# Performance work log

Hardware: AMD Instinct MI355X
Metric: run time of the kernel (lower is better)

## Reference

```python
import jax, jax.numpy as jnp
import numpy as np

B, S, D, H = 2, 1024, 768, 12
HD = D // H          # head_dim = 64
DFF = 4 * D          # 3072
EPS = 1e-5


def _ln(x, g, b):
    m = x.mean(-1, keepdims=True)
    v = ((x - m) ** 2).mean(-1, keepdims=True)
    return (x - m) * jax.lax.rsqrt(v + EPS) * g + b


def setup_inputs() -> dict:
    key = jax.random.key(0)
    ks = jax.random.split(key, 8)
    w = lambda k, shape: jax.random.normal(k, shape, jnp.float32) * 0.02
    return {
        "inp": jax.random.normal(ks[0], (B, S, D), jnp.float32),
        "attention_mask": jnp.zeros((B, S), bool),  # True = masked out (filled with -inf)
        "rel_matrix": jax.random.randint(ks[1], (B, S, S), -1, 2, jnp.int32),  # values in {-1,0,1}
        "qkv_w": w(ks[2], (3 * D, D)),
        "rel_A": w(ks[3], (3, HD)),        # relative_position_emb_A.weight
        "o_w": w(ks[4], (D, D)),
        "w1": w(ks[5], (DFF, D)), "b1": jnp.zeros((DFF,), jnp.float32),
        "w2": w(ks[6], (D, DFF)), "b2": jnp.zeros((D,), jnp.float32),
        "ln1_g": jnp.ones((D,), jnp.float32), "ln1_b": jnp.zeros((D,), jnp.float32),
        "ln2_g": jnp.ones((D,), jnp.float32), "ln2_b": jnp.zeros((D,), jnp.float32),
    }


def reference(inp, attention_mask, rel_matrix, qkv_w, rel_A, o_w,
              w1, b1, w2, b2, ln1_g, ln1_b, ln2_g, ln2_b):
    x = _ln(inp, ln1_g, ln1_b)
    qkv = x @ qkv_w.T                                  # (B,S,3D)
    q, k, v = jnp.split(qkv, 3, axis=-1)
    heads = lambda t: t.reshape(B, S, H, HD).transpose(0, 2, 1, 3)  # (B,H,S,HD)
    q, k, v = heads(q), heads(k), heads(v)

    # q @ (k + rel_emb)^T without materializing k_aug:
    # q.k^T term plus per-(q,key) relative term gathered from q @ A^T.
    logits = jnp.einsum("bhqd,bhkd->bhqk", q, k)       # (B,H,S,S)
    r = jnp.einsum("bhqd,cd->bhqc", q, rel_A)          # (B,H,S,3)
    idx = (rel_matrix + 1).astype(jnp.int32)           # (B,S,S) in {0,1,2}
    rel = jnp.take_along_axis(r, jnp.broadcast_to(idx[:, None], (B, H, S, S)), axis=-1)
    logits = (logits + rel) / np.sqrt(HD).astype(np.float32)
    # masked_fill: -inf where mask is True
    logits = jnp.where(attention_mask[:, None, None, :], -jnp.inf, logits)

    attn = jax.nn.softmax(logits, axis=-1)
    out = jnp.einsum("bhqk,bhkd->bhqd", attn, v)
    out = out.transpose(0, 2, 1, 3).reshape(B, S, D)
    inp = inp + out @ o_w.T                            # residual (dropout=0)

    h = _ln(inp, ln2_g, ln2_b)
    mlp = jax.nn.relu(h @ w1.T + b1) @ w2.T + b2
    return inp + mlp
```

## Files before the change

### kernel.cpp

```cpp
#include <hip/hip_runtime.h>
#include <hip/hip_bf16.h>

#define BB 2
#define SS 1024
#define DD 768
#define HH 12
#define HD 64
#define DFF 3072
#define EPS 1e-5f
#define BS2 (BB * SS)
#define BSD ((size_t)BS2 * DD)

typedef unsigned short ushort_t;
typedef unsigned char uchar_t;
using short8 = __attribute__((ext_vector_type(8))) short;
using f32x4  = __attribute__((ext_vector_type(4))) float;

#define WAITCNT_LGKM0 0xC07F

__device__ __forceinline__ ushort_t f2bf_rne(float f) {
    union { float f; unsigned u; } x; x.f = f;
    unsigned r = x.u + 0x7fff + ((x.u >> 16) & 1);
    return (ushort_t)(r >> 16);
}
__device__ __forceinline__ float bf2f(short u) {
    union { unsigned i; float f; } x;
    x.i = ((unsigned)(ushort_t)u) << 16;
    return x.f;
}
__device__ __forceinline__ short8 mergeo(short8 a, short8 b, float inv) {
    short8 o;
#pragma unroll
    for (int i = 0; i < 8; ++i)
        o[i] = (short)f2bf_rne((bf2f(a[i]) + bf2f(b[i])) * inv);
    return o;
}

__device__ __forceinline__ void cvt_quad(const float* __restrict__ src, int off,
                                         ushort_t* __restrict__ dst, int i) {
    float4 v = ((const float4*)src)[off];
    ushort4 o;
    o.x = f2bf_rne(v.x); o.y = f2bf_rne(v.y);
    o.z = f2bf_rne(v.z); o.w = f2bf_rne(v.w);
    ((ushort4*)dst)[i] = o;
}

#define P1_CVT (3 * DD * DD / 4 / 256)
#define P1_LN  BS2

__global__ __launch_bounds__(256) void prep1_kernel(
    const float* __restrict__ qkv_w, ushort_t* __restrict__ qkvw_bf,
    const float* __restrict__ x, const float* __restrict__ g,
    const float* __restrict__ b, ushort_t* __restrict__ y)
{
    const int bx = blockIdx.x;
    const int t  = threadIdx.x;
    if (bx < P1_CVT) {
        int i = bx * 256 + t;
        cvt_quad(qkv_w, i, qkvw_bf, i);
        return;
    }
    const int row = bx - P1_CVT;
    const float* xr = x + (size_t)row * DD;
    float s = 0.f, ss = 0.f;
    for (int i = t; i < DD; i += 256) {
        float v = xr[i];
        s += v; ss += v * v;
    }
    for (int off = 32; off; off >>= 1) {
        s  += __shfl_down(s,  off);
        ss += __shfl_down(ss, off);
    }
    __shared__ float reds[4], redss[4], bc[2];
    if ((t & 63) == 0) { reds[t >> 6] = s; redss[t >> 6] = ss; }
    __syncthreads();
    if (t == 0) {
        float S1 = reds[0] + reds[1] + reds[2] + reds[3];
        float S2 = redss[0] + redss[1] + redss[2] + redss[3];
        float mean = S1 / DD;
        float var = S2 / DD - mean * mean;
        bc[0] = mean;
        bc[1] = rsqrtf(var + EPS);
    }
    __syncthreads();
    float mean = bc[0], inv = bc[1];
    ushort_t* yr = y + (size_t)row * DD;
    for (int i = t; i < DD; i += 256) {
        yr[i] = f2bf_rne((xr[i] - mean) * inv * g[i] + b[i]);
    }
}

__global__ __launch_bounds__(256) void merge2_ln_kernel(
    const ushort_t* __restrict__ part, const float* __restrict__ inp,
    const float* __restrict__ g, const float* __restrict__ b,
    float* __restrict__ resid, ushort_t* __restrict__ h_bf)
{
    const int row = blockIdx.x;
    const int t = threadIdx.x;
    float4 v = make_float4(0.f, 0.f, 0.f, 0.f);
    const size_t idx = (size_t)row * (DD / 4) + t;
    if (t < DD / 4) {
        v = ((const float4*)inp)[idx];
        ushort4 p0 = ((const ushort4*)part)[idx];
        ushort4 p1 = ((const ushort4*)(part + BSD))[idx];
        v.x += bf2f(p0.x) + bf2f(p1.x);
        v.y += bf2f(p0.y) + bf2f(p1.y);
        v.z += bf2f(p0.z) + bf2f(p1.z);
        v.w += bf2f(p0.w) + bf2f(p1.w);
        ((float4*)resid)[idx] = v;
    }
    float s  = v.x + v.y + v.z + v.w;
    float ss = v.x * v.x + v.y * v.y + v.z * v.z + v.w * v.w;
    for (int off = 32; off; off >>= 1) {
        s  += __shfl_down(s,  off);
        ss += __shfl_down(ss, off);
    }
    __shared__ float reds[4], redss[4], bc[2];
    if ((t & 63) == 0) { reds[t >> 6] = s; redss[t >> 6] = ss; }
    __syncthreads();
    if (t == 0) {
        float S1 = reds[0] + reds[1] + reds[2] + reds[3];
        float S2 = redss[0] + redss[1] + redss[2] + redss[3];
        float mean = S1 / DD;
        float var = S2 / DD - mean * mean;
        bc[0] = mean;
        bc[1] = rsqrtf(var + EPS);
    }
    __syncthreads();
    if (t < DD / 4) {
        const float mean = bc[0], inv = bc[1];
        float4 gv = ((const float4*)g)[t];
        float4 bv = ((const float4*)b)[t];
        ushort4 o;
        o.x = f2bf_rne((v.x - mean) * inv * gv.x + bv.x);
        o.y = f2bf_rne((v.y - mean) * inv * gv.y + bv.y);
        o.z = f2bf_rne((v.z - mean) * inv * gv.z + bv.z);
        o.w = f2bf_rne((v.w - mean) * inv * gv.w + bv.w);
        ((ushort4*)h_bf)[idx] = o;
    }
}

__global__ __launch_bounds__(256) void merge4_kernel(
    const ushort_t* __restrict__ part, const float* __restrict__ resid,
    const float* __restrict__ b2, float* __restrict__ outp, int n4)
{
    int i = blockIdx.x * 256 + threadIdx.x;
    if (i >= n4) return;
    float4 v = ((const float4*)resid)[i];
    int col4 = (i * 4) % DD;
    float4 bv = *(const float4*)(b2 + col4);
    v.x += bv.x; v.y += bv.y; v.z += bv.z; v.w += bv.w;
#pragma unroll
    for (int z = 0; z < 4; ++z) {
        ushort4 pz = ((const ushort4*)(part + (size_t)z * BSD))[i];
        v.x += bf2f(pz.x); v.y += bf2f(pz.y);
        v.z += bf2f(pz.z); v.w += bf2f(pz.w);
    }
    ((float4*)outp)[i] = v;
}

template <bool RELU, bool OUT_BF16, bool HAS_BIAS, bool PARTIAL, bool FUSE_ATT>
__device__ __forceinline__ void gemm_body(
    int bid, int nwg,
    const ushort_t* __restrict__ A, const ushort_t* __restrict__ W,
    const float* __restrict__ bias, void* __restrict__ Cout,
    const float* __restrict__ lpart,
    int M, int N, int K, int Ksplit, int nx)
{
    __shared__ __align__(16) ushort_t As[512 * 8];
    __shared__ __align__(16) ushort_t Bs[1024 * 8];

    const int swz = (bid & 7) * (nwg >> 3) + (bid >> 3);
    const int by  = swz & 31;
    const int t2  = swz >> 5;
    const int bxx = t2 % nx;
    const int bz  = t2 / nx;

    const int t  = threadIdx.x;
    const int n0 = bxx * 128;
    const int m0 = by * 64;
    const int kb = bz * Ksplit;
    const int w  = t >> 6;
    const int l  = t & 63;
    const int wm = (w & 1) * 32;
    const int wn = (w >> 1) * 64;
    const int l15  = l & 15;
    const int quad = l >> 4;

    const ushort_t* gA = A + (size_t)(m0 + (t & 63)) * K + kb + (t >> 6) * 8;
    const ushort_t* gB = W + (size_t)(n0 + (t & 127)) * K + kb + (t >> 7) * 8;

    const float* lp0 = nullptr; const float* lp1 = nullptr;
    const int hbase = kb >> 6;
    if (FUSE_ATT) {
        lp0 = lpart + (size_t)(m0 + (t & 63)) * HH;
        lp1 = lp0 + (size_t)BS2 * HH;
    }

    short8 pa0, pa1, ra0, ra1, sa0, sa1;
    float li0 = 0.f, li1 = 0.f;
    if (FUSE_ATT) {
        ra0 = *(const short8*)(gA);
        ra1 = *(const short8*)(gA + 32);
        sa0 = *(const short8*)(gA + BSD);
        sa1 = *(const short8*)(gA + BSD + 32);
        li0 = lp0[hbase];
        li1 = lp1[hbase];
    } else {
        pa0 = *(const short8*)(gA);
        pa1 = *(const short8*)(gA + 32);
    }
    short8 pb0 = *(const short8*)(gB);
    short8 pb1 = *(const short8*)(gB + 16);
    short8 pb2 = *(const short8*)(gB + 32);
    short8 pb3 = *(const short8*)(gB + 48);

    f32x4 acc[2][4] = {};
    const int nIter = Ksplit >> 6;

    for (int it = 0; it < nIter; ++it) {
        __builtin_amdgcn_s_barrier();
        if (FUSE_ATT) {
            const float inv = 1.0f / (li0 + li1);
            pa0 = mergeo(ra0, sa0, inv);
            pa1 = mergeo(ra1, sa1, inv);
        }
        *(short8*)&As[(size_t)t * 8]           = pa0;
        *(short8*)&As[(size_t)(t + 256) * 8]   = pa1;
        *(short8*)&Bs[(size_t)t * 8]           = pb0;
        *(short8*)&Bs[(size_t)(t + 256) * 8]   = pb1;
        *(short8*)&Bs[(size_t)(t + 512) * 8]   = pb2;
        *(short8*)&Bs[(size_t)(t + 768) * 8]   = pb3;
        if (it + 1 < nIter) {
            const int k0 = (it + 1) << 6;
            if (FUSE_ATT) {
                ra0 = *(const short8*)(gA + k0);
                ra1 = *(const short8*)(gA + k0 + 32);
                sa0 = *(const short8*)(gA + k0 + BSD);
                sa1 = *(const short8*)(gA + k0 + BSD + 32);
                li0 = lp0[hbase + it + 1];
                li1 = lp1[hbase + it + 1];
            } else {
                pa0 = *(const short8*)(gA + k0);
                pa1 = *(const short8*)(gA + k0 + 32);
            }
            pb0 = *(const short8*)(gB + k0);
            pb1 = *(const short8*)(gB + k0 + 16);
            pb2 = *(const short8*)(gB + k0 + 32);
            pb3 = *(const short8*)(gB + k0 + 48);
        }
        __builtin_amdgcn_s_waitcnt(WAITCNT_LGKM0);
        __builtin_amdgcn_s_barrier();

#pragma unroll
        for (int ks = 0; ks < 2; ++ks) {
            const ushort_t* aptr = &As[(size_t)((ks * 4 + quad) * 64 + wm + l15) * 8];
            const ushort_t* bptr = &Bs[(size_t)((ks * 4 + quad) * 128 + wn + l15) * 8];
            short8 af[2], bf[4];
#pragma unroll
            for (int i = 0; i < 2; ++i)
                af[i] = *(const short8*)(aptr + (size_t)i * 16 * 8);
#pragma unroll
            for (int j = 0; j < 4; ++j)
                bf[j] = *(const short8*)(bptr + (size_t)j * 16 * 8);
#pragma unroll
            for (int i = 0; i < 2; ++i)
#pragma unroll
                for (int j = 0; j < 4; ++j)
                    acc[i][j] = __builtin_amdgcn_mfma_f32_16x16x32_bf16(
                        af[i], bf[j], acc[i][j], 0, 0, 0);
        }
    }

    if (PARTIAL) {
        ushort_t* Cp = (ushort_t*)Cout + (size_t)bz * ((size_t)M * N);
#pragma unroll
        for (int i = 0; i < 2; ++i) {
            const int row = m0 + wm + i * 16 + quad * 4;
#pragma unroll
            for (int j = 0; j < 4; ++j) {
                const int col = n0 + wn + j * 16 + l15;
#pragma unroll
                for (int r = 0; r < 4; ++r)
                    Cp[(size_t)(row + r) * N + col] = f2bf_rne(acc[i][j][r]);
            }
        }
    } else {
#pragma unroll
        for (int i = 0; i < 2; ++i) {
            const int row = m0 + wm + i * 16 + quad * 4;
#pragma unroll
            for (int j = 0; j < 4; ++j) {
                const int col = n0 + wn + j * 16 + l15;
                const float bv = HAS_BIAS ? bias[col] : 0.f;
#pragma unroll
                for (int r = 0; r < 4; ++r) {
                    float v = acc[i][j][r] + bv;
                    if (RELU) v = fmaxf(v, 0.f);
                    if (OUT_BF16)
                        ((ushort_t*)Cout)[(size_t)(row + r) * N + col] = f2bf_rne(v);
                    else
                        ((float*)Cout)[(size_t)(row + r) * N + col] = v;
                }
            }
        }
    }
}

template <bool RELU, bool OUT_BF16, bool HAS_BIAS, bool PARTIAL, bool FUSE_ATT>
__global__ __launch_bounds__(256) void gemm_tile(
    const ushort_t* __restrict__ A, const ushort_t* __restrict__ W,
    const float* __restrict__ bias, void* __restrict__ Cout,
    const float* __restrict__ lpart,
    int M, int N, int K, int Ksplit, int nx)
{
    gemm_body<RELU, OUT_BF16, HAS_BIAS, PARTIAL, FUSE_ATT>(
        blockIdx.x, gridDim.x, A, W, bias, Cout, lpart, M, N, K, Ksplit, nx);
}

#define QKV_G (3 * DD / 128 * 32)

__global__ __launch_bounds__(256) void qkv_codes_kernel(
    const ushort_t* __restrict__ A, const ushort_t* __restrict__ W,
    ushort_t* __restrict__ Cout,
    const int* __restrict__ rel, const uchar_t* __restrict__ mask,
    unsigned* __restrict__ codes)
{
    const int bx = blockIdx.x;
    if (bx < QKV_G) {
        gemm_body<false, true, false, false, false>(
            bx, QKV_G, A, W, nullptr, Cout, nullptr,
            BS2, 3 * DD, DD, DD, 3 * DD / 128);
        return;
    }
    const int t = threadIdx.x;
    int tid = (bx - QKV_G) * 256 + t;
    int l15 = tid & 15;
    int kt  = (tid >> 4) & 15;
    int q   = (tid >> 8) & (SS - 1);
    int bb  = tid >> 18;
    const int* rrow = rel + ((size_t)(bb * SS + q)) * SS + kt * 64 + l15;
    const uchar_t* mrow = mask + (size_t)bb * SS + kt * 64 + l15;
    unsigned o = 0;
#pragma unroll
    for (int nt = 0; nt < 4; ++nt) {
        unsigned c = mrow[nt * 16] ? 3u : (unsigned)(rrow[nt * 16] + 1);
        o |= c << (8 * nt);
    }
    codes[((size_t)(bb * SS + q) * 16 + kt) * 16 + l15] = o;
}

#define ATT_G (BB * HH * 16 * 2)
#define RC1 (DD * DD / 4)
#define RC2 (RC1 + DFF * DD / 4)
#define RCT (RC2 + DD * DFF / 4)
#define RCVT_BLK (RCT / 256)

__global__ __launch_bounds__(256) void attn_cvt_kernel(
    const ushort_t* __restrict__ qkv,
    const unsigned* __restrict__ codes,
    const float* __restrict__ rel_A,
    ushort_t* __restrict__ Opart,
    float* __restrict__ lpart,
    const float* __restrict__ o_w, const float* __restrict__ w1,
    const float* __restrict__ w2, ushort_t* __restrict__ wrest)
{
    const int bx = blockIdx.x;
    const int t  = threadIdx.x;
    if (bx >= ATT_G) {
        int i = (bx - ATT_G) * 256 + t;
        const float* src; int off;
        if (i < RC1)      { src = o_w; off = i; }
        else if (i < RC2) { src = w1;  off = i - RC1; }
        else              { src = w2;  off = i - RC2; }
        cvt_quad(src, off, wrest, i);
        return;
    }

    __shared__ __align__(16) ushort_t Ks[2][64 * 64];
    __shared__ __align__(16) unsigned Vt2[2][64 * 36];
    __shared__ __align__(16) ushort_t Ps[64 * 72];
    __shared__ __align__(16) float r3s[64][4];

    const int ks = bx & 1;
    const int qt = (bx >> 1) & 15;
    const int h  = (bx >> 5) % HH;
    const int b  = bx / (32 * HH);
    const int q0 = qt * 64;
    const int w  = t >> 6;
    const int l  = t & 63;
    const int l15  = l & 15;
    const int quad = l >> 4;

    const int sr  = t >> 3;
    const int scp = t & 7;
    const int vkp = t >> 3;
    const int vdg = t & 7;
    const int vkps = vkp ^ (vdg * 4);

    const size_t qrow = (size_t)(b * SS + q0 + w * 16 + l15) * (3 * DD) + h * HD;
    const short8 qf0 = *(const short8*)(qkv + qrow + quad * 8);
    const short8 qf1 = *(const short8*)(qkv + qrow + 32 + quad * 8);

    {
        float rv[3];
#pragma unroll
        for (int c = 0; c < 3; ++c) {
            const float* a = rel_A + c * HD + quad * 8;
            float acc = 0.f;
#pragma unroll
            for (int j = 0; j < 8; ++j) acc += bf2f(qf0[j]) * a[j];
#pragma unroll
            for (int j = 0; j < 8; ++j) acc += bf2f(qf1[j]) * a[32 + j];
            acc += __shfl_xor(acc, 16);
            acc += __shfl_xor(acc, 32);
            rv[c] = acc;
        }
        if (quad == 0) {
            float4 f4 = make_float4(rv[0], rv[1], rv[2], -2.4e31f);
            *(float4*)&r3s[w * 16 + l15][0] = f4;
        }
    }

    float l_run[4] = {0.f, 0.f, 0.f, 0.f};
    f32x4 oacc[4] = {};

    const int kt0 = ks * 8;
    short8 va, vb;
    {
        const int k0 = kt0 * 64;
        const int cl  = scp ^ (sr & 7);
        const ushort_t* g = qkv + (size_t)(b * SS + k0 + sr) * (3 * DD) + DD + h * HD + cl * 8;
        __builtin_amdgcn_global_load_lds(
            (const __attribute__((address_space(1))) unsigned*)g,
            (__attribute__((address_space(3))) unsigned*)(&Ks[0][0] + (size_t)t * 8), 16, 0, 0);
        const int r2  = sr + 32;
        const int cl2 = scp ^ (r2 & 7);
        const ushort_t* g2 = qkv + (size_t)(b * SS + k0 + r2) * (3 * DD) + DD + h * HD + cl2 * 8;
        __builtin_amdgcn_global_load_lds(
            (const __attribute__((address_space(1))) unsigned*)g2,
            (__attribute__((address_space(3))) unsigned*)(&Ks[0][0] + (size_t)(t + 256) * 8), 16, 0, 0);
        const ushort_t* gv = qkv + (size_t)(b * SS + k0 + 2 * vkp) * (3 * DD) + 2 * DD + h * HD + vdg * 8;
        va = *(const short8*)gv;
        vb = *(const short8*)(gv + 3 * DD);
#pragma unroll
        for (int i = 0; i < 8; ++i)
            Vt2[0][(size_t)(vdg * 8 + i) * 36 + vkps] =
                (unsigned)(ushort_t)va[i] | ((unsigned)(ushort_t)vb[i] << 16);
    }
    __syncthreads();
    float4 r3v[4];
#pragma unroll
    for (int reg = 0; reg < 4; ++reg)
        r3v[reg] = *(const float4*)&r3s[w * 16 + quad * 4 + reg][0];

    for (int i8 = 0; i8 < 8; ++i8) {
        const int kt  = kt0 + i8;
        const int cur = i8 & 1;
        const bool more = (i8 + 1 < 8);
        if (more) {
            const int k0 = (kt + 1) * 64;
            const int nb = cur ^ 1;
            const int cl  = scp ^ (sr & 7);
            const ushort_t* g = qkv + (size_t)(b * SS + k0 + sr) * (3 * DD) + DD + h * HD + cl * 8;
            __builtin_amdgcn_global_load_lds(
                (const __attribute__((address_space(1))) unsigned*)g,
                (__attribute__((address_space(3))) unsigned*)(&Ks[nb][0] + (size_t)t * 8), 16, 0, 0);
            const int r2  = sr + 32;
            const int cl2 = scp ^ (r2 & 7);
            const ushort_t* g2 = qkv + (size_t)(b * SS + k0 + r2) * (3 * DD) + DD + h * HD + cl2 * 8;
            __builtin_amdgcn_global_load_lds(
                (const __attribute__((address_space(1))) unsigned*)g2,
                (__attribute__((address_space(3))) unsigned*)(&Ks[nb][0] + (size_t)(t + 256) * 8), 16, 0, 0);
            const ushort_t* gv = qkv + (size_t)(b * SS + k0 + 2 * vkp) * (3 * DD) + 2 * DD + h * HD + vdg * 8;
            va = *(const short8*)gv;
            vb = *(const short8*)(gv + 3 * DD);
        }

        f32x4 sacc[4] = {};
#pragma unroll
        for (int kc = 0; kc < 2; ++kc) {
            const short8 qv = kc ? qf1 : qf0;
#pragma unroll
            for (int nt = 0; nt < 4; ++nt) {
                const int row = nt * 16 + l15;
                const int cp  = (kc * 4 + quad) ^ (row & 7);
                const short8 kf = *(const short8*)(&Ks[cur][0] + (size_t)row * 64 + cp * 8);
                sacc[nt] = __builtin_amdgcn_mfma_f32_16x16x32_bf16(qv, kf, sacc[nt], 0, 0, 0);
            }
        }

#pragma unroll
        for (int reg = 0; reg < 4; ++reg) {
            const int qloc = w * 16 + quad * 4 + reg;
            const unsigned cds = codes[((size_t)(b * SS + q0 + qloc) * 16 + kt) * 16 + l15];
            const float4 r4 = r3v[reg];
#pragma unroll
            for (int nt = 0; nt < 4; ++nt) {
                const unsigned c = (cds >> (8 * nt)) & 0xff;
                float rvv = (c == 0) ? r4.x : (c == 1) ? r4.y : (c == 2) ? r4.z : r4.w;
                const float p = __expf((sacc[nt][reg] + rvv) * 0.125f);
                l_run[reg] += p;
                Ps[(size_t)qloc * 72 + nt * 16 + l15] = f2bf_rne(p);
            }
        }

#pragma unroll
        for (int kc = 0; kc < 2; ++kc) {
            const short8 pf = *(const short8*)(Ps + (size_t)(w * 16 + l15) * 72 + kc * 32 + quad * 8);
#pragma unroll
            for (int dt = 0; dt < 4; ++dt) {
                const int d  = dt * 16 + l15;
                const int dg = d >> 3;
                const int kps0 = (kc * 16 + quad * 4) ^ ((dg & 7) * 4);
                const short8 vf = *(const short8*)((const ushort_t*)&Vt2[cur][(size_t)d * 36 + kps0]);
                oacc[dt] = __builtin_amdgcn_mfma_f32_16x16x32_bf16(pf, vf, oacc[dt], 0, 0, 0);
            }
        }

        if (more) {
            const int nb = cur ^ 1;
#pragma unroll
            for (int i = 0; i < 8; ++i)
                Vt2[nb][(size_t)(vdg * 8 + i) * 36 + vkps] =
                    (unsigned)(ushort_t)va[i] | ((unsigned)(ushort_t)vb[i] << 16);
            __syncthreads();
        }
    }

    ushort_t* Op = Opart + (size_t)ks * BSD;
    float* lp = lpart + (size_t)ks * BS2 * HH;
#pragma unroll
    for (int reg = 0; reg < 4; ++reg) {
        float ls = l_run[reg];
        ls += __shfl_xor(ls, 1);
        ls += __shfl_xor(ls, 2);
        ls += __shfl_xor(ls, 4);
        ls += __shfl_xor(ls, 8);
        const int orow = b * SS + q0 + w * 16 + quad * 4 + reg;
#pragma unroll
        for (int dt = 0; dt < 4; ++dt)
            Op[(size_t)orow * DD + h * HD + dt * 16 + l15] = f2bf_rne(oacc[dt][reg]);
        if (l15 == 0) lp[(size_t)orow * HH + h] = ls;
    }
}

extern "C" void kernel_launch(void* const* d_in, const int* in_sizes, int n_in,
                              void* d_out, int out_size, void* d_ws, size_t ws_size,
                              hipStream_t stream) {
    const float* inp   = (const float*)d_in[0];
    const uchar_t* amask = (const uchar_t*)d_in[1];
    const int*   relm  = (const int*)d_in[2];
    const float* qkv_w = (const float*)d_in[3];
    const float* rel_A = (const float*)d_in[4];
    const float* o_w   = (const float*)d_in[5];
    const float* w1    = (const float*)d_in[6];
    const float* b1    = (const float*)d_in[7];
    const float* w2    = (const float*)d_in[8];
    const float* b2    = (const float*)d_in[9];
    const float* ln1_g = (const float*)d_in[10];
    const float* ln1_b = (const float*)d_in[11];
    const float* ln2_g = (const float*)d_in[12];
    const float* ln2_b = (const float*)d_in[13];
    float* out = (float*)d_out;

    char* p = (char*)d_ws;
    ushort_t* x_bf   = (ushort_t*)p; p += BSD * 2;
    ushort_t* h_bf   = (ushort_t*)p; p += BSD * 2;
    ushort_t* ff_bf  = (ushort_t*)p; p += (size_t)BS2 * DFF * 2;
    ushort_t* qkvw_bf= (ushort_t*)p; p += (size_t)3 * DD * DD * 2;
    ushort_t* ow_bf  = (ushort_t*)p; p += (size_t)DD * DD * 2;
    ushort_t* w1_bf  = (ushort_t*)p; p += (size_t)DFF * DD * 2;
    ushort_t* w2_bf  = (ushort_t*)p; p += (size_t)DD * DFF * 2;
    ushort_t* qkv_bf = (ushort_t*)p; p += (size_t)BS2 * 3 * DD * 2;
    float*    resid  = (float*)p;    p += BSD * 4;
    ushort_t* pool   = (ushort_t*)p; p += 4 * BSD * 2;
    ushort_t* Opart  = (ushort_t*)p; p += 2 * BSD * 2;
    float*    lpart  = (float*)p;    p += (size_t)2 * BS2 * HH * 4;
    unsigned* codes  = (unsigned*)p; p += (size_t)BB * SS * SS;

    prep1_kernel<<<P1_CVT + P1_LN, 256, 0, stream>>>(
        qkv_w, qkvw_bf, inp, ln1_g, ln1_b, x_bf);

    qkv_codes_kernel<<<QKV_G + BB * SS, 256, 0, stream>>>(
        x_bf, qkvw_bf, qkv_bf, relm, amask, codes);

    attn_cvt_kernel<<<ATT_G + RCVT_BLK, 256, 0, stream>>>(
        qkv_bf, codes, rel_A, Opart, lpart, o_w, w1, w2, ow_bf);

    gemm_tile<false, false, false, true, true>
        <<<DD / 128 * 32 * 2, 256, 0, stream>>>(
        Opart, ow_bf, nullptr, pool, lpart, BS2, DD, DD, DD / 2, DD / 128);

    merge2_ln_kernel<<<BS2, 256, 0, stream>>>(
        pool, inp, ln2_g, ln2_b, resid, h_bf);

    gemm_tile<true, true, true, false, false>
        <<<DFF / 128 * 32, 256, 0, stream>>>(
        h_bf, w1_bf, b1, ff_bf, nullptr, BS2, DFF, DD, DD, DFF / 128);

    gemm_tile<false, false, false, true, false>
        <<<DD / 128 * 32 * 4, 256, 0, stream>>>(
        ff_bf, w2_bf, nullptr, pool, nullptr, BS2, DD, DFF, DFF / 4, DD / 128);

    merge4_kernel<<<(int)(BSD / 4 / 256), 256, 0, stream>>>(
        pool, resid, b2, out, (int)(BSD / 4));
}
```

Measured before the change: 253.8 us.

## Fuse all stages into one persistent megakernel with software grid barriers

After: 1.002 ms. +294.9%, slower.

```diff
diff --git a/kernel.cpp b/kernel.cpp
--- a/kernel.cpp
+++ b/kernel.cpp
@@ -11,6 +11,8 @@
 #define BS2 (BB * SS)
 #define BSD ((size_t)BS2 * DD)
 
+#define NBLK 768
+
 typedef unsigned short ushort_t;
 typedef unsigned char uchar_t;
 using short8 = __attribute__((ext_vector_type(8))) short;
@@ -35,7 +37,6 @@
         o[i] = (short)f2bf_rne((bf2f(a[i]) + bf2f(b[i])) * inv);
     return o;
 }
-
 __device__ __forceinline__ void cvt_quad(const float* __restrict__ src, int off,
                                          ushort_t* __restrict__ dst, int i) {
     float4 v = ((const float4*)src)[off];
@@ -45,131 +46,31 @@
     ((ushort4*)dst)[i] = o;
 }
 
-#define P1_CVT (3 * DD * DD / 4 / 256)
-#define P1_LN  BS2
-
-__global__ __launch_bounds__(256) void prep1_kernel(
-    const float* __restrict__ qkv_w, ushort_t* __restrict__ qkvw_bf,
-    const float* __restrict__ x, const float* __restrict__ g,
-    const float* __restrict__ b, ushort_t* __restrict__ y)
-{
-    const int bx = blockIdx.x;
-    const int t  = threadIdx.x;
-    if (bx < P1_CVT) {
-        int i = bx * 256 + t;
-        cvt_quad(qkv_w, i, qkvw_bf, i);
-        return;
-    }
-    const int row = bx - P1_CVT;
-    const float* xr = x + (size_t)row * DD;
-    float s = 0.f, ss = 0.f;
-    for (int i = t; i < DD; i += 256) {
-        float v = xr[i];
-        s += v; ss += v * v;
-    }
-    for (int off = 32; off; off >>= 1) {
-        s  += __shfl_down(s,  off);
-        ss += __shfl_down(ss, off);
-    }
-    __shared__ float reds[4], redss[4], bc[2];
-    if ((t & 63) == 0) { reds[t >> 6] = s; redss[t >> 6] = ss; }
-    __syncthreads();
-    if (t == 0) {
-        float S1 = reds[0] + reds[1] + reds[2] + reds[3];
-        float S2 = redss[0] + redss[1] + redss[2] + redss[3];
-        float mean = S1 / DD;
-        float var = S2 / DD - mean * mean;
-        bc[0] = mean;
-        bc[1] = rsqrtf(var + EPS);
-    }
-    __syncthreads();
-    float mean = bc[0], inv = bc[1];
-    ushort_t* yr = y + (size_t)row * DD;
-    for (int i = t; i < DD; i += 256) {
-        yr[i] = f2bf_rne((xr[i] - mean) * inv * g[i] + b[i]);
-    }
-}
-
-__global__ __launch_bounds__(256) void merge2_ln_kernel(
-    const ushort_t* __restrict__ part, const float* __restrict__ inp,
-    const float* __restrict__ g, const float* __restrict__ b,
-    float* __restrict__ resid, ushort_t* __restrict__ h_bf)
-{
-    const int row = blockIdx.x;
-    const int t = threadIdx.x;
-    float4 v = make_float4(0.f, 0.f, 0.f, 0.f);
-    const size_t idx = (size_t)row * (DD / 4) + t;
-    if (t < DD / 4) {
-        v = ((const float4*)inp)[idx];
-        ushort4 p0 = ((const ushort4*)part)[idx];
-        ushort4 p1 = ((const ushort4*)(part + BSD))[idx];
-        v.x += bf2f(p0.x) + bf2f(p1.x);
-        v.y += bf2f(p0.y) + bf2f(p1.y);
-        v.z += bf2f(p0.z) + bf2f(p1.z);
-        v.w += bf2f(p0.w) + bf2f(p1.w);
-        ((float4*)resid)[idx] = v;
-    }
-    float s  = v.x + v.y + v.z + v.w;
-    float ss = v.x * v.x + v.y * v.y + v.z * v.z + v.w * v.w;
-    for (int off = 32; off; off >>= 1) {
-        s  += __shfl_down(s,  off);
-        ss += __shfl_down(ss, off);
-    }
-    __shared__ float reds[4], redss[4], bc[2];
-    if ((t & 63) == 0) { reds[t >> 6] = s; redss[t >> 6] = ss; }
-    __syncthreads();
-    if (t == 0) {
-        float S1 = reds[0] + reds[1] + reds[2] + reds[3];
-        float S2 = redss[0] + redss[1] + redss[2] + redss[3];
-        float mean = S1 / DD;
-        float var = S2 / DD - mean * mean;
-        bc[0] = mean;
-        bc[1] = rsqrtf(var + EPS);
-    }
-    __syncthreads();
-    if (t < DD / 4) {
-        const float mean = bc[0], inv = bc[1];
-        float4 gv = ((const float4*)g)[t];
-        float4 bv = ((const float4*)b)[t];
-        ushort4 o;
-        o.x = f2bf_rne((v.x - mean) * inv * gv.x + bv.x);
-        o.y = f2bf_rne((v.y - mean) * inv * gv.y + bv.y);
-        o.z = f2bf_rne((v.z - mean) * inv * gv.z + bv.z);
-        o.w = f2bf_rne((v.w - mean) * inv * gv.w + bv.w);
-        ((ushort4*)h_bf)[idx] = o;
-    }
-}
-
-__global__ __launch_bounds__(256) void merge4_kernel(
-    const ushort_t* __restrict__ part, const float* __restrict__ resid,
-    const float* __restrict__ b2, float* __restrict__ outp, int n4)
-{
-    int i = blockIdx.x * 256 + threadIdx.x;
-    if (i >= n4) return;
-    float4 v = ((const float4*)resid)[i];
-    int col4 = (i * 4) % DD;
-    float4 bv = *(const float4*)(b2 + col4);
-    v.x += bv.x; v.y += bv.y; v.z += bv.z; v.w += bv.w;
-#pragma unroll
-    for (int z = 0; z < 4; ++z) {
-        ushort4 pz = ((const ushort4*)(part + (size_t)z * BSD))[i];
-        v.x += bf2f(pz.x); v.y += bf2f(pz.y);
-        v.z += bf2f(pz.z); v.w += bf2f(pz.w);
-    }
-    ((float4*)outp)[i] = v;
+__device__ __forceinline__ void grid_sync(unsigned* bar) {
+    __syncthreads();
+    if (threadIdx.x == 0) {
+        __threadfence();
+        unsigned gen = atomicAdd(bar + 1, 0u);
+        if (atomicAdd(bar, 1u) == NBLK - 1u) {
+            atomicExch(bar, 0u);
+            __threadfence();
+            atomicAdd(bar + 1, 1u);
+        } else {
+            while (atomicAdd(bar + 1, 0u) == gen)
+                __builtin_amdgcn_s_sleep(2);
+            __threadfence();
+        }
+    }
+    __syncthreads();
 }
 
 template <bool RELU, bool OUT_BF16, bool HAS_BIAS, bool PARTIAL, bool FUSE_ATT>
 __device__ __forceinline__ void gemm_body(
-    int bid, int nwg,
-    const ushort_t* __restrict__ A, const ushort_t* __restrict__ W,
-    const float* __restrict__ bias, void* __restrict__ Cout,
-    const float* __restrict__ lpart,
+    int bid, int nwg, ushort_t* As, ushort_t* Bs,
+    const ushort_t* A, const ushort_t* W,
+    const float* bias, void* Cout, const float* lpart,
     int M, int N, int K, int Ksplit, int nx)
 {
-    __shared__ __align__(16) ushort_t As[512 * 8];
-    __shared__ __align__(16) ushort_t Bs[1024 * 8];
-
     const int swz = (bid & 7) * (nwg >> 3) + (bid >> 3);
     const int by  = swz & 31;
     const int t2  = swz >> 5;
@@ -307,86 +208,22 @@
     }
 }
 
-template <bool RELU, bool OUT_BF16, bool HAS_BIAS, bool PARTIAL, bool FUSE_ATT>
-__global__ __launch_bounds__(256) void gemm_tile(
-    const ushort_t* __restrict__ A, const ushort_t* __restrict__ W,
-    const float* __restrict__ bias, void* __restrict__ Cout,
-    const float* __restrict__ lpart,
-    int M, int N, int K, int Ksplit, int nx)
+__device__ __forceinline__ void attn_body(
+    int bx, char* smem,
+    const ushort_t* qkv, const unsigned* codes, const float* rel_A,
+    ushort_t* Opart, float* lpart)
 {
-    gemm_body<RELU, OUT_BF16, HAS_BIAS, PARTIAL, FUSE_ATT>(
-        blockIdx.x, gridDim.x, A, W, bias, Cout, lpart, M, N, K, Ksplit, nx);
-}
-
-#define QKV_G (3 * DD / 128 * 32)
-
-__global__ __launch_bounds__(256) void qkv_codes_kernel(
-    const ushort_t* __restrict__ A, const ushort_t* __restrict__ W,
-    ushort_t* __restrict__ Cout,
-    const int* __restrict__ rel, const uchar_t* __restrict__ mask,
-    unsigned* __restrict__ codes)
-{
-    const int bx = blockIdx.x;
-    if (bx < QKV_G) {
-        gemm_body<false, true, false, false, false>(
-            bx, QKV_G, A, W, nullptr, Cout, nullptr,
-            BS2, 3 * DD, DD, DD, 3 * DD / 128);
-        return;
-    }
-    const int t = threadIdx.x;
-    int tid = (bx - QKV_G) * 256 + t;
-    int l15 = tid & 15;
-    int kt  = (tid >> 4) & 15;
-    int q   = (tid >> 8) & (SS - 1);
-    int bb  = tid >> 18;
-    const int* rrow = rel + ((size_t)(bb * SS + q)) * SS + kt * 64 + l15;
-    const uchar_t* mrow = mask + (size_t)bb * SS + kt * 64 + l15;
-    unsigned o = 0;
-#pragma unroll
-    for (int nt = 0; nt < 4; ++nt) {
-        unsigned c = mrow[nt * 16] ? 3u : (unsigned)(rrow[nt * 16] + 1);
-        o |= c << (8 * nt);
-    }
-    codes[((size_t)(bb * SS + q) * 16 + kt) * 16 + l15] = o;
-}
-
-#define ATT_G (BB * HH * 16 * 2)
-#define RC1 (DD * DD / 4)
-#define RC2 (RC1 + DFF * DD / 4)
-#define RCT (RC2 + DD * DFF / 4)
-#define RCVT_BLK (RCT / 256)
-
-__global__ __launch_bounds__(256) void attn_cvt_kernel(
-    const ushort_t* __restrict__ qkv,
-    const unsigned* __restrict__ codes,
-    const float* __restrict__ rel_A,
-    ushort_t* __restrict__ Opart,
-    float* __restrict__ lpart,
-    const float* __restrict__ o_w, const float* __restrict__ w1,
-    const float* __restrict__ w2, ushort_t* __restrict__ wrest)
-{
-    const int bx = blockIdx.x;
-    const int t  = threadIdx.x;
-    if (bx >= ATT_G) {
-        int i = (bx - ATT_G) * 256 + t;
-        const float* src; int off;
-        if (i < RC1)      { src = o_w; off = i; }
-        else if (i < RC2) { src = w1;  off = i - RC1; }
-        else              { src = w2;  off = i - RC2; }
-        cvt_quad(src, off, wrest, i);
-        return;
-    }
-
-    __shared__ __align__(16) ushort_t Ks[2][64 * 64];
-    __shared__ __align__(16) unsigned Vt2[2][64 * 36];
-    __shared__ __align__(16) ushort_t Ps[64 * 72];
-    __shared__ __align__(16) float r3s[64][4];
+    ushort_t* Ks0 = (ushort_t*)smem;
+    unsigned* Vt0 = (unsigned*)(smem + 16384);
+    ushort_t* Psp = (ushort_t*)(smem + 34816);
+    float*    r3p = (float*)(smem + 44032);
 
     const int ks = bx & 1;
     const int qt = (bx >> 1) & 15;
     const int h  = (bx >> 5) % HH;
     const int b  = bx / (32 * HH);
     const int q0 = qt * 64;
+    const int t  = threadIdx.x;
     const int w  = t >> 6;
     const int l  = t & 63;
     const int l15  = l & 15;
@@ -418,7 +255,7 @@
         }
         if (quad == 0) {
             float4 f4 = make_float4(rv[0], rv[1], rv[2], -2.4e31f);
-            *(float4*)&r3s[w * 16 + l15][0] = f4;
+            *(float4*)&r3p[(w * 16 + l15) * 4] = f4;
         }
     }
 
@@ -433,26 +270,26 @@
         const ushort_t* g = qkv + (size_t)(b * SS + k0 + sr) * (3 * DD) + DD + h * HD + cl * 8;
         __builtin_amdgcn_global_load_lds(
             (const __attribute__((address_space(1))) unsigned*)g,
-            (__attribute__((address_space(3))) unsigned*)(&Ks[0][0] + (size_t)t * 8), 16, 0, 0);
+            (__attribute__((address_space(3))) unsigned*)(Ks0 + (size_t)t * 8), 16, 0, 0);
         const int r2  = sr + 32;
         const int cl2 = scp ^ (r2 & 7);
         const ushort_t* g2 = qkv + (size_t)(b * SS + k0 + r2) * (3 * DD) + DD + h * HD + cl2 * 8;
         __builtin_amdgcn_global_load_lds(
             (const __attribute__((address_space(1))) unsigned*)g2,
-            (__attribute__((address_space(3))) unsigned*)(&Ks[0][0] + (size_t)(t + 256) * 8), 16, 0, 0);
+            (__attribute__((address_space(3))) unsigned*)(Ks0 + (size_t)(t + 256) * 8), 16, 0, 0);
         const ushort_t* gv = qkv + (size_t)(b * SS + k0 + 2 * vkp) * (3 * DD) + 2 * DD + h * HD + vdg * 8;
         va = *(const short8*)gv;
         vb = *(const short8*)(gv + 3 * DD);
 #pragma unroll
         for (int i = 0; i < 8; ++i)
-            Vt2[0][(size_t)(vdg * 8 + i) * 36 + vkps] =
+            Vt0[(size_t)(vdg * 8 + i) * 36 + vkps] =
                 (unsigned)(ushort_t)va[i] | ((unsigned)(ushort_t)vb[i] << 16);
     }
     __syncthreads();
     float4 r3v[4];
 #pragma unroll
     for (int reg = 0; reg < 4; ++reg)
-        r3v[reg] = *(const float4*)&r3s[w * 16 + quad * 4 + reg][0];
+        r3v[reg] = *(const float4*)&r3p[(w * 16 + quad * 4 + reg) * 4];
 
     for (int i8 = 0; i8 < 8; ++i8) {
         const int kt  = kt0 + i8;
@@ -465,13 +302,13 @@
             const ushort_t* g = qkv + (size_t)(b * SS + k0 + sr) * (3 * DD) + DD + h * HD + cl * 8;
             __builtin_amdgcn_global_load_lds(
                 (const __attribute__((address_space(1))) unsigned*)g,
-                (__attribute__((address_space(3))) unsigned*)(&Ks[nb][0] + (size_t)t * 8), 16, 0, 0);
+                (__attribute__((address_space(3))) unsigned*)(Ks0 + nb * 4096 + (size_t)t * 8), 16, 0, 0);
             const int r2  = sr + 32;
             const int cl2 = scp ^ (r2 & 7);
             const ushort_t* g2 = qkv + (size_t)(b * SS + k0 + r2) * (3 * DD) + DD + h * HD + cl2 * 8;
             __builtin_amdgcn_global_load_lds(
                 (const __attribute__((address_space(1))) unsigned*)g2,
-                (__attribute__((address_space(3))) unsigned*)(&Ks[nb][0] + (size_t)(t + 256) * 8), 16, 0, 0);
+                (__attribute__((address_space(3))) unsigned*)(Ks0 + nb * 4096 + (size_t)(t + 256) * 8), 16, 0, 0);
             const ushort_t* gv = qkv + (size_t)(b * SS + k0 + 2 * vkp) * (3 * DD) + 2 * DD + h * HD + vdg * 8;
             va = *(const short8*)gv;
             vb = *(const short8*)(gv + 3 * DD);
@@ -485,7 +322,7 @@
             for (int nt = 0; nt < 4; ++nt) {
                 const int row = nt * 16 + l15;
                 const int cp  = (kc * 4 + quad) ^ (row & 7);
-                const short8 kf = *(const short8*)(&Ks[cur][0] + (size_t)row * 64 + cp * 8);
+                const short8 kf = *(const short8*)(Ks0 + cur * 4096 + (size_t)row * 64 + cp * 8);
                 sacc[nt] = __builtin_amdgcn_mfma_f32_16x16x32_bf16(qv, kf, sacc[nt], 0, 0, 0);
             }
         }
@@ -501,19 +338,19 @@
                 float rvv = (c == 0) ? r4.x : (c == 1) ? r4.y : (c == 2) ? r4.z : r4.w;
                 const float p = __expf((sacc[nt][reg] + rvv) * 0.125f);
                 l_run[reg] += p;
-                Ps[(size_t)qloc * 72 + nt * 16 + l15] = f2bf_rne(p);
+                Psp[(size_t)qloc * 72 + nt * 16 + l15] = f2bf_rne(p);
             }
         }
 
 #pragma unroll
         for (int kc = 0; kc < 2; ++kc) {
-            const short8 pf = *(const short8*)(Ps + (size_t)(w * 16 + l15) * 72 + kc * 32 + quad * 8);
+            const short8 pf = *(const short8*)(Psp + (size_t)(w * 16 + l15) * 72 + kc * 32 + quad * 8);
 #pragma unroll
             for (int dt = 0; dt < 4; ++dt) {
                 const int d  = dt * 16 + l15;
                 const int dg = d >> 3;
                 const int kps0 = (kc * 16 + quad * 4) ^ ((dg & 7) * 4);
-                const short8 vf = *(const short8*)((const ushort_t*)&Vt2[cur][(size_t)d * 36 + kps0]);
+                const short8 vf = *(const short8*)((const ushort_t*)&Vt0[cur * 2304 + (size_t)d * 36 + kps0]);
                 oacc[dt] = __builtin_amdgcn_mfma_f32_16x16x32_bf16(pf, vf, oacc[dt], 0, 0, 0);
             }
         }
@@ -522,7 +359,7 @@
             const int nb = cur ^ 1;
 #pragma unroll
             for (int i = 0; i < 8; ++i)
-                Vt2[nb][(size_t)(vdg * 8 + i) * 36 + vkps] =
+                Vt0[nb * 2304 + (size_t)(vdg * 8 + i) * 36 + vkps] =
                     (unsigned)(ushort_t)va[i] | ((unsigned)(ushort_t)vb[i] << 16);
             __syncthreads();
         }
@@ -542,6 +379,207 @@
         for (int dt = 0; dt < 4; ++dt)
             Op[(size_t)orow * DD + h * HD + dt * 16 + l15] = f2bf_rne(oacc[dt][reg]);
         if (l15 == 0) lp[(size_t)orow * HH + h] = ls;
+    }
+}
+
+__device__ __forceinline__ void ln_row(
+    int row, int t, const float* x, const float* g, const float* b,
+    ushort_t* y, char* smem)
+{
+    float* reds  = (float*)smem;
+    float* redss = reds + 4;
+    float* bc    = redss + 4;
+    const float* xr = x + (size_t)row * DD;
+    float s = 0.f, ss = 0.f;
+    for (int i = t; i < DD; i += 256) {
+        float v = xr[i];
+        s += v; ss += v * v;
+    }
+    for (int off = 32; off; off >>= 1) {
+        s  += __shfl_down(s,  off);
+        ss += __shfl_down(ss, off);
+    }
+    if ((t & 63) == 0) { reds[t >> 6] = s; redss[t >> 6] = ss; }
+    __syncthreads();
+    if (t == 0) {
+        float S1 = reds[0] + reds[1] + reds[2] + reds[3];
+        float S2 = redss[0] + redss[1] + redss[2] + redss[3];
+        float mean = S1 / DD;
+        float var = S2 / DD - mean * mean;
+        bc[0] = mean;
+        bc[1] = rsqrtf(var + EPS);
+    }
+    __syncthreads();
+    float mean = bc[0], inv = bc[1];
+    ushort_t* yr = y + (size_t)row * DD;
+    for (int i = t; i < DD; i += 256)
+        yr[i] = f2bf_rne((xr[i] - mean) * inv * g[i] + b[i]);
+    __syncthreads();
+}
+
+__device__ __forceinline__ void m2ln_row(
+    int row, int t, const ushort_t* part, const float* inp,
+    const float* g, const float* b, float* resid, ushort_t* h_bf, char* smem)
+{
+    float* reds  = (float*)smem;
+    float* redss = reds + 4;
+    float* bc    = redss + 4;
+    float4 v = make_float4(0.f, 0.f, 0.f, 0.f);
+    const size_t idx = (size_t)row * (DD / 4) + t;
+    if (t < DD / 4) {
+        v = ((const float4*)inp)[idx];
+        ushort4 p0 = ((const ushort4*)part)[idx];
+        ushort4 p1 = ((const ushort4*)(part + BSD))[idx];
+        v.x += bf2f(p0.x) + bf2f(p1.x);
+        v.y += bf2f(p0.y) + bf2f(p1.y);
+        v.z += bf2f(p0.z) + bf2f(p1.z);
+        v.w += bf2f(p0.w) + bf2f(p1.w);
+        ((float4*)resid)[idx] = v;
+    }
+    float s  = v.x + v.y + v.z + v.w;
+    float ss = v.x * v.x + v.y * v.y + v.z * v.z + v.w * v.w;
+    for (int off = 32; off; off >>= 1) {
+        s  += __shfl_down(s,  off);
+        ss += __shfl_down(ss, off);
+    }
+    if ((t & 63) == 0) { reds[t >> 6] = s; redss[t >> 6] = ss; }
+    __syncthreads();
+    if (t == 0) {
+        float S1 = reds[0] + reds[1] + reds[2] + reds[3];
+        float S2 = redss[0] + redss[1] + redss[2] + redss[3];
+        float mean = S1 / DD;
+        float var = S2 / DD - mean * mean;
+        bc[0] = mean;
+        bc[1] = rsqrtf(var + EPS);
+    }
+    __syncthreads();
+    if (t < DD / 4) {
+        const float mean = bc[0], inv = bc[1];
+        float4 gv = ((const float4*)g)[t];
+        float4 bv = ((const float4*)b)[t];
+        ushort4 o;
+        o.x = f2bf_rne((v.x - mean) * inv * gv.x + bv.x);
+        o.y = f2bf_rne((v.y - mean) * inv * gv.y + bv.y);
+        o.z = f2bf_rne((v.z - mean) * inv * gv.z + bv.z);
+        o.w = f2bf_rne((v.w - mean) * inv * gv.w + bv.w);
+        ((ushort4*)h_bf)[idx] = o;
+    }
+    __syncthreads();
+}
+
+__device__ __forceinline__ void codes_unit(
+    int cu, int t, const int* rel, const uchar_t* mask, unsigned* codes)
+{
+    int tid = cu * 256 + t;
+    int l15 = tid & 15;
+    int kt  = (tid >> 4) & 15;
+    int q   = (tid >> 8) & (SS - 1);
+    int bb  = tid >> 18;
+    const int* rrow = rel + ((size_t)(bb * SS + q)) * SS + kt * 64 + l15;
+    const uchar_t* mrow = mask + (size_t)bb * SS + kt * 64 + l15;
+    unsigned o = 0;
+#pragma unroll
+    for (int nt = 0; nt < 4; ++nt) {
+        unsigned c = mrow[nt * 16] ? 3u : (unsigned)(rrow[nt * 16] + 1);
+        o |= c << (8 * nt);
+    }
+    codes[((size_t)(bb * SS + q) * 16 + kt) * 16 + l15] = o;
+}
+
+#define P_CVT1  1728
+#define P_LN    (P_CVT1 + BS2)
+#define P_CODES (P_LN + BS2)
+#define RC1 (DD * DD / 4)
+#define RC2 (RC1 + DFF * DD / 4)
+#define P_TOT   (P_CODES + 5184)
+
+__global__ __launch_bounds__(256, 3) void mega_kernel(
+    const float* inp, const uchar_t* amask, const int* relm,
+    const float* qkv_w, const float* rel_A, const float* o_w,
+    const float* w1, const float* b1, const float* w2, const float* b2,
+    const float* ln1_g, const float* ln1_b, const float* ln2_g, const float* ln2_b,
+    float* out, char* ws)
+{
+    __shared__ __align__(16) char smem[45056];
+    ushort_t* As = (ushort_t*)smem;
+    ushort_t* Bs = (ushort_t*)(smem + 8192);
+
+    char* p = ws;
+    ushort_t* x_bf   = (ushort_t*)p; p += BSD * 2;
+    ushort_t* h_bf   = (ushort_t*)p; p += BSD * 2;
+    ushort_t* ff_bf  = (ushort_t*)p; p += (size_t)BS2 * DFF * 2;
+    ushort_t* qkvw_bf= (ushort_t*)p; p += (size_t)3 * DD * DD * 2;
+    ushort_t* ow_bf  = (ushort_t*)p; p += (size_t)DD * DD * 2;
+    ushort_t* w1_bf  = (ushort_t*)p; p += (size_t)DFF * DD * 2;
+    ushort_t* w2_bf  = (ushort_t*)p; p += (size_t)DD * DFF * 2;
+    ushort_t* qkv_bf = (ushort_t*)p; p += (size_t)BS2 * 3 * DD * 2;
+    float*    resid  = (float*)p;    p += BSD * 4;
+    ushort_t* pool   = (ushort_t*)p; p += 4 * BSD * 2;
+    ushort_t* Opart  = (ushort_t*)p; p += 2 * BSD * 2;
+    float*    lpart  = (float*)p;    p += (size_t)2 * BS2 * HH * 4;
+    unsigned* codes  = (unsigned*)p; p += (size_t)BB * SS * SS;
+    unsigned* gbar   = (unsigned*)p;
+
+    const int bid = blockIdx.x;
+    const int t   = threadIdx.x;
+
+    for (int u = bid; u < P_TOT; u += NBLK) {
+        if (u < P_CVT1) {
+            int i = u * 256 + t;
+            cvt_quad(qkv_w, i, qkvw_bf, i);
+        } else if (u < P_LN) {
+            ln_row(u - P_CVT1, t, inp, ln1_g, ln1_b, x_bf, smem);
+        } else if (u < P_CODES) {
+            codes_unit(u - P_LN, t, relm, amask, codes);
+        } else {
+            int i = (u - P_CODES) * 256 + t;
+            const float* src; int off;
+            if (i < RC1)      { src = o_w; off = i; }
+            else if (i < RC2) { src = w1;  off = i - RC1; }
+            else              { src = w2;  off = i - RC2; }
+            cvt_quad(src, off, ow_bf, i);
+        }
+    }
+    grid_sync(gbar);
+
+    if (bid < 576)
+        gemm_body<false, true, false, false, false>(bid, 576, As, Bs,
+            x_bf, qkvw_bf, nullptr, qkv_bf, nullptr, BS2, 3 * DD, DD, DD, 18);
+    grid_sync(gbar);
+
+    attn_body(bid, smem, qkv_bf, codes, rel_A, Opart, lpart);
+    grid_sync(gbar);
+
+    if (bid < 384)
+        gemm_body<false, false, false, true, true>(bid, 384, As, Bs,
+            Opart, ow_bf, nullptr, pool, lpart, BS2, DD, DD, DD / 2, 6);
+    grid_sync(gbar);
+
+    for (int row = bid; row < BS2; row += NBLK)
+        m2ln_row(row, t, pool, inp, ln2_g, ln2_b, resid, h_bf, smem);
+    grid_sync(gbar);
+
+    gemm_body<true, true, true, false, false>(bid, 768, As, Bs,
+        h_bf, w1_bf, b1, ff_bf, nullptr, BS2, DFF, DD, DD, 24);
+    grid_sync(gbar);
+
+    gemm_body<false, false, false, true, false>(bid, 768, As, Bs,
+        ff_bf, w2_bf, nullptr, pool, nullptr, BS2, DD, DFF, DFF / 4, 6);
+    grid_sync(gbar);
+
+    for (int u = bid; u < 1536; u += NBLK) {
+        int i = u * 256 + t;
+        float4 v = ((const float4*)resid)[i];
+        int col4 = (i * 4) % DD;
+        float4 bv = *(const float4*)(b2 + col4);
+        v.x += bv.x; v.y += bv.y; v.z += bv.z; v.w += bv.w;
+#pragma unroll
+        for (int z = 0; z < 4; ++z) {
+            ushort4 pz = ((const ushort4*)(pool + (size_t)z * BSD))[i];
+            v.x += bf2f(pz.x); v.y += bf2f(pz.y);
+            v.z += bf2f(pz.z); v.w += bf2f(pz.w);
+        }
+        ((float4*)out)[i] = v;
     }
 }
 
@@ -565,44 +603,24 @@
     float* out = (float*)d_out;
 
     char* p = (char*)d_ws;
-    ushort_t* x_bf   = (ushort_t*)p; p += BSD * 2;
-    ushort_t* h_bf   = (ushort_t*)p; p += BSD * 2;
-    ushort_t* ff_bf  = (ushort_t*)p; p += (size_t)BS2 * DFF * 2;
-    ushort_t* qkvw_bf= (ushort_t*)p; p += (size_t)3 * DD * DD * 2;
-    ushort_t* ow_bf  = (ushort_t*)p; p += (size_t)DD * DD * 2;
-    ushort_t* w1_bf  = (ushort_t*)p; p += (size_t)DFF * DD * 2;
-    ushort_t* w2_bf  = (ushort_t*)p; p += (size_t)DD * DFF * 2;
-    ushort_t* qkv_bf = (ushort_t*)p; p += (size_t)BS2 * 3 * DD * 2;
-    float*    resid  = (float*)p;    p += BSD * 4;
-    ushort_t* pool   = (ushort_t*)p; p += 4 * BSD * 2;
-    ushort_t* Opart  = (ushort_t*)p; p += 2 * BSD * 2;
-    float*    lpart  = (float*)p;    p += (size_t)2 * BS2 * HH * 4;
-    unsigned* codes  = (unsigned*)p; p += (size_t)BB * SS * SS;
-
-    prep1_kernel<<<P1_CVT + P1_LN, 256, 0, stream>>>(
-        qkv_w, qkvw_bf, inp, ln1_g, ln1_b, x_bf);
-
-    qkv_codes_kernel<<<QKV_G + BB * SS, 256, 0, stream>>>(
-        x_bf, qkvw_bf, qkv_bf, relm, amask, codes);
-
-    attn_cvt_kernel<<<ATT_G + RCVT_BLK, 256, 0, stream>>>(
-        qkv_bf, codes, rel_A, Opart, lpart, o_w, w1, w2, ow_bf);
-
-    gemm_tile<false, false, false, true, true>
-        <<<DD / 128 * 32 * 2, 256, 0, stream>>>(
-        Opart, ow_bf, nullptr, pool, lpart, BS2, DD, DD, DD / 2, DD / 128);
-
-    merge2_ln_kernel<<<BS2, 256, 0, stream>>>(
-        pool, inp, ln2_g, ln2_b, resid, h_bf);
-
-    gemm_tile<true, true, true, false, false>
-        <<<DFF / 128 * 32, 256, 0, stream>>>(
-        h_bf, w1_bf, b1, ff_bf, nullptr, BS2, DFF, DD, DD, DFF / 128);
-
-    gemm_tile<false, false, false, true, false>
-        <<<DD / 128 * 32 * 4, 256, 0, stream>>>(
-        ff_bf, w2_bf, nullptr, pool, nullptr, BS2, DD, DFF, DFF / 4, DD / 128);
-
-    merge4_kernel<<<(int)(BSD / 4 / 256), 256, 0, stream>>>(
-        pool, resid, b2, out, (int)(BSD / 4));
-}
+    p += BSD * 2;
+    p += BSD * 2;
+    p += (size_t)BS2 * DFF * 2;
+    p += (size_t)3 * DD * DD * 2;
+    p += (size_t)DD * DD * 2;
+    p += (size_t)DFF * DD * 2;
+    p += (size_t)DD * DFF * 2;
+    p += (size_t)BS2 * 3 * DD * 2;
+    p += BSD * 4;
+    p += 4 * BSD * 2;
+    p += 2 * BSD * 2;
+    p += (size_t)2 * BS2 * HH * 4;
+    p += (size_t)BB * SS * SS;
+    unsigned* gbar = (unsigned*)p;
+
+    hipMemsetAsync(gbar, 0, 64, stream);
+
+    mega_kernel<<<NBLK, 256, 0, stream>>>(
+        inp, amask, relm, qkv_w, rel_A, o_w, w1, b1, w2, b2,
+        ln1_g, ln1_b, ln2_g, ln2_b, out, (char*)d_ws);
+}
```
